# Optimization experiments

Measured on AMD Instinct MI355X. Metric: run time of the kernel, lower is better.

## Reference

```python
import jax, jax.numpy as jnp
import numpy as np

EMBED = 1024
NUM_EXPERTS = 8
ACTIVE = 2
HIDDEN = 4 * EMBED


def setup_inputs() -> dict:
    key = jax.random.key(0)
    ks = jax.random.split(key, 7)
    B, T = 4, 1024
    s1 = 1.0 / np.sqrt(EMBED)
    s2 = 1.0 / np.sqrt(HIDDEN)
    return {
        "x": jax.random.normal(ks[0], (B, T, EMBED), dtype=jnp.float32),
        # stacked expert weights, layout [in, out] (torch Linear applies x @ W.T + b)
        "W1": jax.random.uniform(ks[1], (NUM_EXPERTS, EMBED, HIDDEN), jnp.float32, -s1, s1),
        "b1": jax.random.uniform(ks[2], (NUM_EXPERTS, HIDDEN), jnp.float32, -s1, s1),
        "W2": jax.random.uniform(ks[3], (NUM_EXPERTS, HIDDEN, EMBED), jnp.float32, -s2, s2),
        "b2": jax.random.uniform(ks[4], (NUM_EXPERTS, EMBED), jnp.float32, -s2, s2),
        "Wr": jax.random.uniform(ks[5], (EMBED, NUM_EXPERTS), jnp.float32, -s1, s1),
        "br": jax.random.uniform(ks[6], (NUM_EXPERTS,), jnp.float32, -s1, s1),
    }


def reference(x, W1, b1, W2, b2, Wr, br):
    # ---- router (TopkRouter) ----
    scores = x @ Wr + br                                  # [B,T,E]
    topk_scores, indices = jax.lax.top_k(scores, ACTIVE)  # [B,T,K]
    # mask = zeros scattered with topk scores at topk positions (others stay 0),
    # then softmax over ALL experts (faithful to the reference's quirky softmax).
    one_hot = jax.nn.one_hot(indices, NUM_EXPERTS, dtype=scores.dtype)  # [B,T,K,E]
    mask = jnp.einsum('btke,btk->bte', one_hot, topk_scores)            # [B,T,E]
    router_output = jax.nn.softmax(mask, axis=-1)                       # [B,T,E]

    # ---- dense all-experts FFN (Expert): relu(x@W1+b1)@W2+b2 per expert ----
    h = jax.nn.relu(jnp.einsum('btd,edh->bteh', x, W1) + b1)            # [B,T,E,H]
    expert_outputs = jnp.einsum('bteh,ehd->bted', h, W2) + b2           # [B,T,E,D]

    # ---- weighted combine ----
    return jnp.einsum('bte,bted->btd', router_output, expert_outputs)   # [B,T,D]
```

## Files before the change

kernel.cpp:

```cpp
#include <hip/hip_runtime.h>
#include <hip/hip_bf16.h>
#include <cstdint>
#include <cstddef>

#define EMBED  1024
#define NEXP   8
#define HIDDEN 4096
#define TOKENS 4096
#define MC     2048

typedef __attribute__((ext_vector_type(8))) short bf16x8;
typedef __attribute__((ext_vector_type(4))) float f32x4;
using bf16 = __hip_bfloat16;

__device__ __forceinline__ void gload_lds16(const void* g, void* l) {
    __builtin_amdgcn_global_load_lds((const __attribute__((address_space(1))) void*)g,
                                     (__attribute__((address_space(3))) void*)l,
                                     16, 0, 0);
}

__device__ __forceinline__ int swzA(int b) { return b ^ (((b >> 7) & 3) << 4); }
__device__ __forceinline__ int swzB(int b) { return b ^ (((b >> 7) & 7) << 4); }

__global__ void cvt_kernel(const float* __restrict__ in, bf16* __restrict__ out, size_t n) {
    size_t i = ((size_t)blockIdx.x * blockDim.x + threadIdx.x) * 4;
    if (i + 3 < n) {
        float4 v = *(const float4*)(in + i);
        out[i + 0] = __float2bfloat16(v.x);
        out[i + 1] = __float2bfloat16(v.y);
        out[i + 2] = __float2bfloat16(v.z);
        out[i + 3] = __float2bfloat16(v.w);
    }
}

__global__ void transpose_cvt(const float* __restrict__ in, bf16* __restrict__ out,
                              int K, int N, size_t in_estride, size_t out_eoff, int ldo) {
    const int e = blockIdx.z;
    const float* ine = in + (size_t)e * in_estride;
    bf16* oute = out + (size_t)e * out_eoff;
    __shared__ float tile[32][33];
    const int n0 = blockIdx.x * 32, k0 = blockIdx.y * 32;
    const int tx = threadIdx.x, ty = threadIdx.y;
    #pragma unroll
    for (int i = ty; i < 32; i += 8)
        tile[i][tx] = ine[(size_t)(k0 + i) * N + n0 + tx];
    __syncthreads();
    #pragma unroll
    for (int i = ty; i < 32; i += 8)
        oute[(size_t)(n0 + i) * ldo + k0 + tx] = __float2bfloat16(tile[tx][i]);
}

__global__ void router_kernel(const float* __restrict__ x, const float* __restrict__ Wr,
                              const float* __restrict__ br, float* __restrict__ w) {
    const int t = blockIdx.x;
    const int lane = threadIdx.x;
    const float* xt = x + (size_t)t * EMBED;
    float s[NEXP];
    #pragma unroll
    for (int e = 0; e < NEXP; e++) s[e] = 0.f;
    for (int k = lane; k < EMBED; k += 64) {
        const float xv = xt[k];
        const float* wrk = Wr + (size_t)k * NEXP;
        #pragma unroll
        for (int e = 0; e < NEXP; e++) s[e] = fmaf(xv, wrk[e], s[e]);
    }
    #pragma unroll
    for (int e = 0; e < NEXP; e++) {
        #pragma unroll
        for (int off = 32; off >= 1; off >>= 1)
            s[e] += __shfl_xor(s[e], off);
    }
    if (lane == 0) {
        float sc[NEXP];
        #pragma unroll
        for (int e = 0; e < NEXP; e++) sc[e] = s[e] + br[e];
        int i1 = 0; float m1 = sc[0];
        #pragma unroll
        for (int e = 1; e < NEXP; e++) if (sc[e] > m1) { m1 = sc[e]; i1 = e; }
        int i2 = -1; float m2 = -1e30f;
        #pragma unroll
        for (int e = 0; e < NEXP; e++) if (e != i1 && sc[e] > m2) { m2 = sc[e]; i2 = e; }
        const float mx = fmaxf(m1, 0.f);
        const float denom = 6.f * expf(0.f - mx) + expf(m1 - mx) + expf(m2 - mx);
        #pragma unroll
        for (int e = 0; e < NEXP; e++) {
            float v = (e == i1) ? m1 : ((e == i2) ? m2 : 0.f);
            w[(size_t)t * NEXP + e] = expf(v - mx) / denom;
        }
    }
}

#define G1_PREAMBLE(Abase, Bbase, lda, ldb)                                              \
    __shared__ __align__(16) bf16 As[3][128 * 32];                                       \
    __shared__ __align__(16) bf16 Bs[3][128 * 32];                                       \
    const int tid = threadIdx.x;                                                         \
    f32x4 acc[4][4] = {};                                                                \
    int srow[2], scol[2];                                                                \
    _Pragma("unroll")                                                                    \
    for (int j = 0; j < 2; j++) {                                                        \
        int b0 = tid * 16 + j * 4096;                                                    \
        int bs = swzA(b0);                                                               \
        srow[j] = bs >> 6; scol[j] = (bs & 63) >> 1;                                     \
    }                                                                                    \
    const bf16* ga0 = (Abase) + (size_t)(brow + srow[0]) * (lda) + scol[0];              \
    const bf16* ga1 = (Abase) + (size_t)(brow + srow[1]) * (lda) + scol[1];              \
    const bf16* gb0 = (Bbase) + (size_t)(bcol + srow[0]) * (ldb) + scol[0];              \
    const bf16* gb1 = (Bbase) + (size_t)(bcol + srow[1]) * (ldb) + scol[1];              \
    const int lane = tid & 63, wid = tid >> 6;                                           \
    const int wv_r = (wid >> 1) * 64, wv_c = (wid & 1) * 64;                             \
    const int fr = lane & 15, kbyte = (lane >> 4) * 16;                                  \
    int offA[4], offB[4];                                                                \
    _Pragma("unroll")                                                                    \
    for (int m = 0; m < 4; m++) {                                                        \
        offA[m] = swzA((wv_r + m * 16 + fr) * 64 + kbyte);                               \
        offB[m] = swzA((wv_c + m * 16 + fr) * 64 + kbyte);                               \
    }

#define G1_STAGE(s, kt)                                                                  \
    do {                                                                                 \
        gload_lds16(ga0 + (kt), &As[s][tid * 8]);                                        \
        gload_lds16(ga1 + (kt), &As[s][tid * 8 + 2048]);                                 \
        gload_lds16(gb0 + (kt), &Bs[s][tid * 8]);                                        \
        gload_lds16(gb1 + (kt), &Bs[s][tid * 8 + 2048]);                                 \
    } while (0)

#define G1_KLOOP(NT)                                                                     \
    G1_STAGE(0, 0);                                                                      \
    G1_STAGE(1, 32);                                                                     \
    {                                                                                    \
        int slot = 0, nslot = 2;                                                         \
        for (int t = 0; t < (NT); ++t) {                                                 \
            if (t + 2 < (NT)) { G1_STAGE(nslot, (t + 2) * 32); }                         \
            if (t < (NT) - 2)       asm volatile("s_waitcnt vmcnt(8)" ::: "memory");     \
            else if (t == (NT) - 2) asm volatile("s_waitcnt vmcnt(4)" ::: "memory");     \
            else                    asm volatile("s_waitcnt vmcnt(0)" ::: "memory");     \
            __builtin_amdgcn_s_barrier();                                                \
            __builtin_amdgcn_sched_barrier(0);                                           \
            const char* Ab = (const char*)As[slot];                                      \
            const char* Bb = (const char*)Bs[slot];                                      \
            bf16x8 af[4], bfr[4];                                                        \
            _Pragma("unroll")                                                            \
            for (int m = 0; m < 4; m++) af[m] = *(const bf16x8*)(Ab + offA[m]);          \
            _Pragma("unroll")                                                            \
            for (int n = 0; n < 4; n++) bfr[n] = *(const bf16x8*)(Bb + offB[n]);         \
            __builtin_amdgcn_s_setprio(1);                                               \
            _Pragma("unroll")                                                            \
            for (int m = 0; m < 4; m++)                                                  \
                _Pragma("unroll")                                                        \
                for (int n = 0; n < 4; n++)                                              \
                    acc[m][n] = __builtin_amdgcn_mfma_f32_16x16x32_bf16(af[m], bfr[n],   \
                                                                       acc[m][n], 0, 0, 0); \
            __builtin_amdgcn_s_setprio(0);                                               \
            asm volatile("" ::: "memory");                                               \
            __builtin_amdgcn_s_barrier();                                                \
            slot = (slot == 2) ? 0 : slot + 1;                                           \
            nslot = (nslot == 2) ? 0 : nslot + 1;                                        \
        }                                                                                \
    }

__global__ __launch_bounds__(256, 3) void gemm1(const bf16* __restrict__ A,
                                                const bf16* __restrict__ Bt,
                                                const float* __restrict__ b1,
                                                const float* __restrict__ rw,
                                                bf16* __restrict__ H) {
    const int wg = blockIdx.x;
    const int sw = (wg & 7) * 512 + (wg >> 3);
    const int e  = sw >> 9;
    const int rem = sw & 511;
    const int brow = (rem >> 5) * 128;
    const int bcol = (rem & 31) * 128;
    const bf16* Be = Bt + (size_t)e * HIDDEN * EMBED;
    bf16* He = H + (size_t)e * MC * HIDDEN;

    G1_PREAMBLE(A, Be, EMBED, EMBED)
    G1_KLOOP(EMBED / 32)

    #pragma unroll
    for (int n = 0; n < 4; n++) {
        const int col = bcol + wv_c + n * 16 + fr;
        const float bias = b1[e * HIDDEN + col];
        #pragma unroll
        for (int m = 0; m < 4; m++) {
            const int rowb = brow + wv_r + m * 16 + (lane >> 4) * 4;
            #pragma unroll
            for (int j = 0; j < 4; j++) {
                const int row = rowb + j;
                float v = acc[m][n][j] + bias;
                v = fmaxf(v, 0.f) * rw[(size_t)row * NEXP + e];
                He[(size_t)row * HIDDEN + col] = __float2bfloat16(v);
            }
        }
    }
}

#define BARX()  { __builtin_amdgcn_sched_barrier(0); __builtin_amdgcn_s_barrier(); __builtin_amdgcn_sched_barrier(0); }
#define LGKM0() { asm volatile("s_waitcnt lgkmcnt(0)" ::: "memory"); __builtin_amdgcn_sched_barrier(0); }

#define PIPE_PREAMBLE(Abase, Bbase, lda, ldb)                                        \
    __shared__ __align__(16) bf16 As[2][2][128 * 64];                                \
    __shared__ __align__(16) bf16 Bs[2][2][128 * 64];                                \
    const int tid = threadIdx.x;                                                     \
    const int lane = tid & 63, wid = tid >> 6;                                       \
    const int mhalf = wid >> 2, wB = wid & 3;                                        \
    const int nhalf = wB >> 1, nsub = wB & 1;                                        \
    const int wv_r = mhalf * 128, wv_c = wB * 64;                                    \
    f32x4 acc[8][4] = {};                                                            \
    int rowloc[2], colel[2];                                                         \
    _Pragma("unroll")                                                                \
    for (int j = 0; j < 2; j++) {                                                    \
        int bs = swzB(tid * 16 + j * 8192);                                          \
        rowloc[j] = bs >> 7; colel[j] = (bs & 127) >> 1;                             \
    }                                                                                \
    const bf16* pA0 = (Abase) + (size_t)(brow + rowloc[0]) * (lda) + colel[0];       \
    const bf16* pA1 = (Abase) + (size_t)(brow + rowloc[1]) * (lda) + colel[1];       \
    const bf16* pB0 = (Bbase) + (size_t)(bcol + rowloc[0]) * (ldb) + colel[0];       \
    const bf16* pB1 = (Bbase) + (size_t)(bcol + rowloc[1]) * (ldb) + colel[1];       \
    const int fr = lane & 15, kb0 = (lane >> 4) * 16;                                \
    const int xm = (fr & 7) << 4;                                                    \
    const int baA0 = (fr * 128 + kb0) ^ xm, baA1 = (fr * 128 + kb0 + 64) ^ xm;       \
    const int brB = (nsub * 64 + fr) * 128;                                          \
    const int baB0 = (brB + kb0) ^ xm, baB1 = (brB + kb0 + 64) ^ xm;

#define STAGE_A(bi, h, koff, lda)                                                    \
    do {                                                                             \
        gload_lds16(pA0 + (size_t)(h) * 128 * (lda) + (koff), &As[bi][h][tid * 8]);  \
        gload_lds16(pA1 + (size_t)(h) * 128 * (lda) + (koff), &As[bi][h][tid * 8 + 4096]); \
    } while (0)
#define STAGE_B(bi, h, koff, ldb)                                                    \
    do {                                                                             \
        gload_lds16(pB0 + (size_t)(h) * 128 * (ldb) + (koff), &Bs[bi][h][tid * 8]);  \
        gload_lds16(pB1 + (size_t)(h) * 128 * (ldb) + (koff), &Bs[bi][h][tid * 8 + 4096]); \
    } while (0)

#define MFMA_Q(mh, nh)                                                               \
    __builtin_amdgcn_s_setprio(1);                                                   \
    _Pragma("unroll")                                                                \
    for (int mm = 0; mm < 4; mm++)                                                   \
        _Pragma("unroll")                                                            \
        for (int nn = 0; nn < 2; nn++) {                                             \
            acc[(mh)*4+mm][(nh)*2+nn] = __builtin_amdgcn_mfma_f32_16x16x32_bf16(     \
                a[(mh)*4+mm][0], b[(nh)*2+nn][0], acc[(mh)*4+mm][(nh)*2+nn], 0,0,0); \
            acc[(mh)*4+mm][(nh)*2+nn] = __builtin_amdgcn_mfma_f32_16x16x32_bf16(     \
                a[(mh)*4+mm][1], b[(nh)*2+nn][1], acc[(mh)*4+mm][(nh)*2+nn], 0,0,0); \
        }                                                                            \
    __builtin_amdgcn_s_setprio(0);

#define PIPE_KLOOP(NT, lda, ldb)                                                     \
    STAGE_A(0, 0, 0, lda); STAGE_A(0, 1, 0, lda);                                    \
    STAGE_B(0, 0, 0, ldb); STAGE_B(0, 1, 0, ldb);                                    \
    STAGE_A(1, 0, 64, lda); STAGE_A(1, 1, 64, lda);                                  \
    STAGE_B(1, 0, 64, ldb); STAGE_B(1, 1, 64, ldb);                                  \
    asm volatile("s_waitcnt vmcnt(8)" ::: "memory");                                 \
    BARX();                                                                          \
    for (int t = 0; t < (NT); ++t) {                                                 \
        const int bi = t & 1;                                                        \
        const bool st = (t + 2) < (NT);                                              \
        const size_t koff = (size_t)(t + 2) * 64;                                    \
        const char* Ah = (const char*)&As[bi][mhalf][0];                             \
        const char* Bh = (const char*)&Bs[bi][nhalf][0];                             \
        bf16x8 a[8][2], b[4][2];                                                     \
                                        \
        _Pragma("unroll")                                                            \
        for (int m = 0; m < 4; m++) {                                                \
            a[m][0] = *(const bf16x8*)(Ah + baA0 + m * 2048);                        \
            a[m][1] = *(const bf16x8*)(Ah + baA1 + m * 2048);                        \
        }                                                                            \
        _Pragma("unroll")                                                            \
        for (int n = 0; n < 2; n++) {                                                \
            b[n][0] = *(const bf16x8*)(Bh + baB0 + n * 2048);                        \
            b[n][1] = *(const bf16x8*)(Bh + baB1 + n * 2048);                        \
        }                                                                            \
        BARX(); LGKM0();                                                             \
        MFMA_Q(0, 0)                                                                 \
                                                   \
        _Pragma("unroll")                                                            \
        for (int n = 2; n < 4; n++) {                                                \
            b[n][0] = *(const bf16x8*)(Bh + baB0 + n * 2048);                        \
            b[n][1] = *(const bf16x8*)(Bh + baB1 + n * 2048);                        \
        }                                                                            \
        BARX(); LGKM0();                                                             \
        MFMA_Q(0, 1)                                                                 \
        BARX();                                                                      \
                                     \
        _Pragma("unroll")                                                            \
        for (int m = 4; m < 8; m++) {                                                \
            a[m][0] = *(const bf16x8*)(Ah + baA0 + m * 2048);                        \
            a[m][1] = *(const bf16x8*)(Ah + baA1 + m * 2048);                        \
        }                                                                            \
        if (st) { STAGE_B(bi, 0, koff, ldb); STAGE_B(bi, 1, koff, ldb); }            \
        BARX(); LGKM0();                                                             \
        MFMA_Q(1, 0)                                                                 \
        BARX();                                                                      \
                       \
        if (st) { STAGE_A(bi, 0, koff, lda); STAGE_A(bi, 1, koff, lda); }            \
        MFMA_Q(1, 1)                                                                 \
        if (st) { asm volatile("s_waitcnt vmcnt(8)" ::: "memory"); }                 \
        else    { asm volatile("s_waitcnt vmcnt(0)" ::: "memory"); }                 \
        BARX();                                                                      \
    }

__global__ __launch_bounds__(512, 2) void gemm2(const bf16* __restrict__ A,
                                                const bf16* __restrict__ Bt,
                                                const float* __restrict__ b2,
                                                const float* __restrict__ rw,
                                                float* __restrict__ out) {
    const int e = blockIdx.z;
    const int brow = blockIdx.y * 256;
    const int bcol = blockIdx.x * 256;
    const bf16* Ae = A + (size_t)e * MC * HIDDEN;
    const bf16* Be = Bt + (size_t)e * EMBED * HIDDEN;

    PIPE_PREAMBLE(Ae, Be, HIDDEN, HIDDEN)
    PIPE_KLOOP(64, HIDDEN, HIDDEN)

    #pragma unroll
    for (int n = 0; n < 4; n++) {
        const int col = bcol + wv_c + n * 16 + fr;
        #pragma unroll
        for (int m = 0; m < 8; m++) {
            const int rowb = brow + wv_r + m * 16 + (lane >> 4) * 4;
            #pragma unroll
            for (int j = 0; j < 4; j++) {
                const int row = rowb + j;
                float v = acc[m][n][j];
                if (e == 0) {
                    const float* wrow = rw + (size_t)row * NEXP;
                    float s = 0.f;
                    #pragma unroll
                    for (int ee = 0; ee < NEXP; ee++) s = fmaf(wrow[ee], b2[ee * EMBED + col], s);
                    v += s;
                }
                atomicAdd(out + (size_t)row * EMBED + col, v);
            }
        }
    }
}

extern "C" void kernel_launch(void* const* d_in, const int* in_sizes, int n_in,
                              void* d_out, int out_size, void* d_ws, size_t ws_size,
                              hipStream_t stream) {
    const float* x  = (const float*)d_in[0];
    const float* W1 = (const float*)d_in[1];
    const float* b1 = (const float*)d_in[2];
    const float* W2 = (const float*)d_in[3];
    const float* b2 = (const float*)d_in[4];
    const float* Wr = (const float*)d_in[5];
    const float* br = (const float*)d_in[6];
    float* out = (float*)d_out;

    uint8_t* ws = (uint8_t*)d_ws;
    size_t off = 0;
    auto walloc = [&](size_t bytes) -> void* {
        void* p = ws + off;
        off += (bytes + 255) & ~(size_t)255;
        return p;
    };
    float* rw  = (float*)walloc((size_t)TOKENS * NEXP * 4);
    bf16* xb   = (bf16*)walloc((size_t)TOKENS * EMBED * 2);
    bf16* w1t  = (bf16*)walloc((size_t)NEXP * HIDDEN * EMBED * 2);
    bf16* w2t  = (bf16*)walloc((size_t)NEXP * EMBED * HIDDEN * 2);
    bf16* hbuf = (bf16*)walloc((size_t)NEXP * MC * HIDDEN * 2);

    hipMemsetAsync(d_out, 0, (size_t)out_size * sizeof(float), stream);

    cvt_kernel<<<4096, 256, 0, stream>>>(x, xb, (size_t)TOKENS * EMBED);

    dim3 tb(32, 8);
    transpose_cvt<<<dim3(HIDDEN / 32, EMBED / 32, NEXP), tb, 0, stream>>>(
        W1, w1t, EMBED, HIDDEN, (size_t)EMBED * HIDDEN, (size_t)HIDDEN * EMBED, EMBED);
    transpose_cvt<<<dim3(EMBED / 32, HIDDEN / 32, NEXP), tb, 0, stream>>>(
        W2, w2t, HIDDEN, EMBED, (size_t)HIDDEN * EMBED, (size_t)EMBED * HIDDEN, HIDDEN);

    router_kernel<<<TOKENS, 64, 0, stream>>>(x, Wr, br, rw);

    for (int m0 = 0; m0 < TOKENS; m0 += MC) {
        gemm1<<<4096, 256, 0, stream>>>(
            xb + (size_t)m0 * EMBED, w1t, b1, rw + (size_t)m0 * NEXP, hbuf);
        gemm2<<<dim3(EMBED / 256, MC / 256, NEXP), 512, 0, stream>>>(
            hbuf, w2t, b2, rw + (size_t)m0 * NEXP, out + (size_t)m0 * EMBED);
    }
}
```

Measured before the change: 955.0 us.

## Run gemm2 once over all tokens with two experts fused per K-chunk

The hidden buffer now holds all tokens, so gemm1 runs in token chunks and writes into the full buffer. gemm2 then launches once over all 4096 tokens, with each block accumulating two experts back to back along K (128 k-tiles), which halves the number of atomic adds into the output. gemm1 drops its swizzled 1D block order for a plain 3D grid. This costs a much larger workspace (twice the hidden buffer) and may lose the cache locality the swizzle gave gemm1.

```diff
diff --git a/kernel.cpp b/kernel.cpp
--- a/kernel.cpp
+++ b/kernel.cpp
@@ -7,7 +7,7 @@
 #define NEXP   8
 #define HIDDEN 4096
 #define TOKENS 4096
-#define MC     2048
+#define MC     1024
 
 typedef __attribute__((ext_vector_type(8))) short bf16x8;
 typedef __attribute__((ext_vector_type(4))) float f32x4;
@@ -163,14 +163,11 @@
                                                 const float* __restrict__ b1,
                                                 const float* __restrict__ rw,
                                                 bf16* __restrict__ H) {
-    const int wg = blockIdx.x;
-    const int sw = (wg & 7) * 512 + (wg >> 3);
-    const int e  = sw >> 9;
-    const int rem = sw & 511;
-    const int brow = (rem >> 5) * 128;
-    const int bcol = (rem & 31) * 128;
+    const int e = blockIdx.z;
+    const int brow = blockIdx.x * 128;
+    const int bcol = blockIdx.y * 128;
     const bf16* Be = Bt + (size_t)e * HIDDEN * EMBED;
-    bf16* He = H + (size_t)e * MC * HIDDEN;
+    bf16* He = H + (size_t)e * TOKENS * HIDDEN;
 
     G1_PREAMBLE(A, Be, EMBED, EMBED)
     G1_KLOOP(EMBED / 32)
@@ -195,6 +192,8 @@
 
 #define BARX()  { __builtin_amdgcn_sched_barrier(0); __builtin_amdgcn_s_barrier(); __builtin_amdgcn_sched_barrier(0); }
 #define LGKM0() { asm volatile("s_waitcnt lgkmcnt(0)" ::: "memory"); __builtin_amdgcn_sched_barrier(0); }
+
+#define KOFF(T, estride) ((size_t)((T) & 63) * 64 + (size_t)((T) >> 6) * (estride))
 
 #define PIPE_PREAMBLE(Abase, Bbase, lda, ldb)                                        \
     __shared__ __align__(16) bf16 As[2][2][128 * 64];                                \
@@ -245,7 +244,7 @@
         }                                                                            \
     __builtin_amdgcn_s_setprio(0);
 
-#define PIPE_KLOOP(NT, lda, ldb)                                                     \
+#define PIPE_KLOOP(NT, lda, ldb, eA, eB)                                             \
     STAGE_A(0, 0, 0, lda); STAGE_A(0, 1, 0, lda);                                    \
     STAGE_B(0, 0, 0, ldb); STAGE_B(0, 1, 0, ldb);                                    \
     STAGE_A(1, 0, 64, lda); STAGE_A(1, 1, 64, lda);                                  \
@@ -255,7 +254,8 @@
     for (int t = 0; t < (NT); ++t) {                                                 \
         const int bi = t & 1;                                                        \
         const bool st = (t + 2) < (NT);                                              \
-        const size_t koff = (size_t)(t + 2) * 64;                                    \
+        const size_t koffA = KOFF(t + 2, eA);                                        \
+        const size_t koffB = KOFF(t + 2, eB);                                        \
         const char* Ah = (const char*)&As[bi][mhalf][0];                             \
         const char* Bh = (const char*)&Bs[bi][nhalf][0];                             \
         bf16x8 a[8][2], b[4][2];                                                     \
@@ -287,12 +287,12 @@
             a[m][0] = *(const bf16x8*)(Ah + baA0 + m * 2048);                        \
             a[m][1] = *(const bf16x8*)(Ah + baA1 + m * 2048);                        \
         }                                                                            \
-        if (st) { STAGE_B(bi, 0, koff, ldb); STAGE_B(bi, 1, koff, ldb); }            \
+        if (st) { STAGE_B(bi, 0, koffB, ldb); STAGE_B(bi, 1, koffB, ldb); }          \
         BARX(); LGKM0();                                                             \
         MFMA_Q(1, 0)                                                                 \
         BARX();                                                                      \
                        \
-        if (st) { STAGE_A(bi, 0, koff, lda); STAGE_A(bi, 1, koff, lda); }            \
+        if (st) { STAGE_A(bi, 0, koffA, lda); STAGE_A(bi, 1, koffA, lda); }          \
         MFMA_Q(1, 1)                                                                 \
         if (st) { asm volatile("s_waitcnt vmcnt(8)" ::: "memory"); }                 \
         else    { asm volatile("s_waitcnt vmcnt(0)" ::: "memory"); }                 \
@@ -304,14 +304,16 @@
                                                 const float* __restrict__ b2,
                                                 const float* __restrict__ rw,
                                                 float* __restrict__ out) {
-    const int e = blockIdx.z;
+    const int kc = blockIdx.z;
     const int brow = blockIdx.y * 256;
     const int bcol = blockIdx.x * 256;
-    const bf16* Ae = A + (size_t)e * MC * HIDDEN;
-    const bf16* Be = Bt + (size_t)e * EMBED * HIDDEN;
+    const size_t eA = (size_t)TOKENS * HIDDEN;
+    const size_t eB = (size_t)EMBED * HIDDEN;
+    const bf16* Ae = A + (size_t)(kc * 2) * eA;
+    const bf16* Be = Bt + (size_t)(kc * 2) * eB;
 
     PIPE_PREAMBLE(Ae, Be, HIDDEN, HIDDEN)
-    PIPE_KLOOP(64, HIDDEN, HIDDEN)
+    PIPE_KLOOP(128, HIDDEN, HIDDEN, eA, eB)
 
     #pragma unroll
     for (int n = 0; n < 4; n++) {
@@ -323,7 +325,7 @@
             for (int j = 0; j < 4; j++) {
                 const int row = rowb + j;
                 float v = acc[m][n][j];
-                if (e == 0) {
+                if (kc == 0) {
                     const float* wrow = rw + (size_t)row * NEXP;
                     float s = 0.f;
                     #pragma unroll
@@ -359,7 +361,7 @@
     bf16* xb   = (bf16*)walloc((size_t)TOKENS * EMBED * 2);
     bf16* w1t  = (bf16*)walloc((size_t)NEXP * HIDDEN * EMBED * 2);
     bf16* w2t  = (bf16*)walloc((size_t)NEXP * EMBED * HIDDEN * 2);
-    bf16* hbuf = (bf16*)walloc((size_t)NEXP * MC * HIDDEN * 2);
+    bf16* hbuf = (bf16*)walloc((size_t)NEXP * TOKENS * HIDDEN * 2);
 
     hipMemsetAsync(d_out, 0, (size_t)out_size * sizeof(float), stream);
 
@@ -374,9 +376,9 @@
     router_kernel<<<TOKENS, 64, 0, stream>>>(x, Wr, br, rw);
 
     for (int m0 = 0; m0 < TOKENS; m0 += MC) {
-        gemm1<<<4096, 256, 0, stream>>>(
-            xb + (size_t)m0 * EMBED, w1t, b1, rw + (size_t)m0 * NEXP, hbuf);
-        gemm2<<<dim3(EMBED / 256, MC / 256, NEXP), 512, 0, stream>>>(
-            hbuf, w2t, b2, rw + (size_t)m0 * NEXP, out + (size_t)m0 * EMBED);
-    }
-}
+        gemm1<<<dim3(MC / 128, HIDDEN / 128, NEXP), 256, 0, stream>>>(
+            xb + (size_t)m0 * EMBED, w1t, b1, rw + (size_t)m0 * NEXP,
+            hbuf + (size_t)m0 * HIDDEN);
+    }
+    gemm2<<<dim3(EMBED / 256, TOKENS / 256, 4), 512, 0, stream>>>(hbuf, w2t, b2, rw, out);
+}
```

Result: faster. 900.1 us (-5.7%).
